# Performance work log

Hardware: AMD Instinct MI355X
Metric: run time of the kernel (lower is better)

## Reference

```python
import jax, jax.numpy as jnp
import numpy as np

B, L = 4096, 64          # batch, patch_len
OUT, KS, K = 64, 8, 4    # out_planes, kernel_size, num mixtures
STRIDE = 1
TEMP = 34.0
L_OUT = (L - KS) // STRIDE + 1   # 57
C = OUT * L_OUT                  # BN feature dim = 3648
HIDDEN = int(L * 0.5) + 1        # attention hidden planes = 33
EPS = 1e-5


def _gelu(x):
    return jax.nn.gelu(x, approximate=False)  # torch nn.GELU default = exact erf


def setup_inputs() -> dict:
    key = jax.random.key(0)
    ks = jax.random.split(key, 8)
    return {
        "x": jax.random.normal(ks[0], (B, L), jnp.float32),
        "fc1_w": jax.random.normal(ks[1], (HIDDEN, L), jnp.float32) * (2.0 / HIDDEN) ** 0.5,
        "fc2_w": jax.random.normal(ks[2], (K, HIDDEN), jnp.float32) * (2.0 / K) ** 0.5,
        "fc2_b": jnp.zeros((K,), jnp.float32),
        "weight": jax.random.normal(ks[3], (K, OUT, KS), jnp.float32) * 0.1,
        "bias": jnp.zeros((K, OUT), jnp.float32),
        "bn_gamma": jnp.ones((C,), jnp.float32),
        "bn_beta": jnp.zeros((C,), jnp.float32),
    }


def reference(x, fc1_w, fc2_w, fc2_b, weight, bias, bn_gamma, bn_beta):
    # --- attention1d: 1x1 convs over the patch_len 'channel' dim == linears ---
    a = _gelu(x @ fc1_w.T)                 # [B, HIDDEN]
    logits = a @ fc2_w.T + fc2_b           # [B, K]
    attn = jax.nn.softmax(logits / TEMP, axis=1)

    # --- sliding windows (im2col), shared by both conv paths ---
    idx = jnp.arange(L_OUT)[:, None] * STRIDE + jnp.arange(KS)[None, :]
    frames = x[:, idx]                     # [B, L_OUT, KS]

    # --- kernel_wise: full conv with each of the K kernels ---
    kw = jnp.einsum('blc,koc->bolk', frames, weight) + bias.T[None, :, None, :]  # [B,OUT,L_OUT,K]
    kw = kw.reshape(B, C, K)

    # --- per-sample aggregated kernel + grouped (per-sample) conv ---
    agg_w = jnp.einsum('bk,koc->boc', attn, weight)      # [B, OUT, KS]
    agg_b = attn @ bias                                  # [B, OUT]
    out = jnp.einsum('blc,boc->bol', frames, agg_w) + agg_b[:, :, None]  # [B,OUT,L_OUT]
    out = out.reshape(B, C)

    # --- BN(GELU(.)) with batch statistics (training-mode BatchNorm1d) ---
    g = _gelu(out)
    m = g.mean(axis=0)
    v = g.var(axis=0)
    out = (g - m) * jax.lax.rsqrt(v + EPS) * bn_gamma + bn_beta

    g2 = _gelu(kw)                                        # [B, C, K]
    m2 = g2.mean(axis=(0, 2), keepdims=True)
    v2 = g2.var(axis=(0, 2), keepdims=True)
    kw = (g2 - m2) * jax.lax.rsqrt(v2 + EPS) * bn_gamma[None, :, None] + bn_beta[None, :, None]

    return out, attn, kw.transpose(0, 2, 1)              # [B,C], [B,K], [B,K,C]
```

## Files before the change

kernel.cpp:

```cpp
#include <hip/hip_runtime.h>
#include <cstddef>

#define B_     4096
#define L_     64
#define OUT_   64
#define KS_    8
#define KK_    4
#define LOUT_  57
#define C_     3648
#define HID_   33
#define TEMP_  34.0f
#define EPS_   1e-5f
#define NCH_   128
#define SROWS_ 32
#define NB2_   32

typedef float f32x2 __attribute__((ext_vector_type(2)));

__device__ __forceinline__ f32x2 pk_fma(f32x2 a, f32x2 b, f32x2 c) {
    return __builtin_elementwise_fma(a, b, c);
}

__device__ __forceinline__ float gelu_f(float x) {
    float e = exp2f(-2.3022083f * x * fmaf(0.044715f * x, x, 1.0f));
    return x * __builtin_amdgcn_rcpf(1.0f + e);
}

__device__ __forceinline__ f32x2 gelu2(f32x2 x) {
    const f32x2 one = {1.f, 1.f};
    const f32x2 ca  = {0.044715f, 0.044715f};
    const f32x2 cb  = {-2.3022083f, -2.3022083f};
    f32x2 t = pk_fma(x * ca, x, one);
    f32x2 u = x * t * cb;
    f32x2 e = {exp2f(u.x), exp2f(u.y)};
    f32x2 d = e + one;
    f32x2 r = {__builtin_amdgcn_rcpf(d.x), __builtin_amdgcn_rcpf(d.y)};
    return x * r;
}

template<int ROWS>
__device__ __forceinline__ void stage_shifted(
    const float* __restrict__ x, int b0, int tid,
    float4 (*xs4)[ROWS][17])
{
    for (int idx = tid; idx < ROWS * 16; idx += 256) {
        int r = idx >> 4, t = idx & 15;
        const float4* xrow = (const float4*)(x + (size_t)(b0 + r) * L_);
        float4 a  = xrow[t];
        float4 bq = xrow[t < 15 ? t + 1 : 15];
        xs4[0][r][t] = a;
        xs4[1][r][t] = make_float4(a.y, a.z, a.w, bq.x);
        xs4[2][r][t] = make_float4(a.z, a.w, bq.x, bq.y);
        xs4[3][r][t] = make_float4(a.w, bq.x, bq.y, bq.z);
    }
}

__global__ __launch_bounds__(128) void attn_kernel(
    const float* __restrict__ x, const float* __restrict__ fc1_w,
    const float* __restrict__ fc2_w, const float* __restrict__ fc2_b,
    float* __restrict__ attn_out)
{
    __shared__ float fc1s[HID_][L_];
    __shared__ float fc2s[KK_][HID_];
    __shared__ float fc2bs[KK_];
    int tid = threadIdx.x;
    for (int i = tid; i < HID_ * L_; i += 128) fc1s[i / L_][i % L_] = fc1_w[i];
    for (int i = tid; i < KK_ * HID_; i += 128) fc2s[i / HID_][i % HID_] = fc2_w[i];
    if (tid < KK_) fc2bs[tid] = fc2_b[tid];
    __syncthreads();

    int b = blockIdx.x * 128 + tid;

    float xr[L_];
    const float4* xp = (const float4*)(x + (size_t)b * L_);
    #pragma unroll
    for (int i = 0; i < L_ / 4; ++i) {
        float4 v = xp[i];
        xr[4*i] = v.x; xr[4*i+1] = v.y; xr[4*i+2] = v.z; xr[4*i+3] = v.w;
    }
    float logit[KK_] = {0.f, 0.f, 0.f, 0.f};
    for (int h = 0; h < HID_; ++h) {
        const float4* fr = (const float4*)&fc1s[h][0];
        float acc = 0.f;
        #pragma unroll
        for (int i = 0; i < L_ / 4; ++i) {
            float4 wv = fr[i];
            acc = fmaf(xr[4*i],   wv.x, acc);
            acc = fmaf(xr[4*i+1], wv.y, acc);
            acc = fmaf(xr[4*i+2], wv.z, acc);
            acc = fmaf(xr[4*i+3], wv.w, acc);
        }
        float a = gelu_f(acc);
        #pragma unroll
        for (int k = 0; k < KK_; ++k) logit[k] = fmaf(a, fc2s[k][h], logit[k]);
    }
    float z[KK_];
    #pragma unroll
    for (int k = 0; k < KK_; ++k) z[k] = (logit[k] + fc2bs[k]) * (1.0f / TEMP_);
    float mx = fmaxf(fmaxf(z[0], z[1]), fmaxf(z[2], z[3]));
    float e[KK_]; float s = 0.f;
    #pragma unroll
    for (int k = 0; k < KK_; ++k) { e[k] = __expf(z[k] - mx); s += e[k]; }
    float inv = __builtin_amdgcn_rcpf(s);
    #pragma unroll
    for (int k = 0; k < KK_; ++k) attn_out[(size_t)b * KK_ + k] = e[k] * inv;
}

__global__ __launch_bounds__(256) void stats_kernel(
    const float* __restrict__ x, const float* __restrict__ weight,
    const float* __restrict__ bias, const float* __restrict__ attn,
    float* __restrict__ P, int use_partial)
{
    int cb = blockIdx.x;
    int chunk = blockIdx.y;
    int tid = threadIdx.x;
    int c = cb * 256 + tid;
    bool act = c < C_;
    int o = act ? (c / LOUT_) : 0;
    int l = act ? (c - o * LOUT_) : 0;
    int q = l >> 2, s = l & 3;

    f32x2 wp[KK_][4];
    float bk[KK_];
    #pragma unroll
    for (int k = 0; k < KK_; ++k) {
        bk[k] = bias[k * OUT_ + o];
        const float* wk = weight + (size_t)(k * OUT_ + o) * KS_;
        #pragma unroll
        for (int j = 0; j < 4; ++j) wp[k][j] = f32x2{wk[2*j], wk[2*j+1]};
    }

    __shared__ float4 xs4[4][SROWS_][17];
    __shared__ float at[SROWS_][KK_];

    int b0 = chunk * SROWS_;
    stage_shifted<SROWS_>(x, b0, tid, xs4);
    if (tid < SROWS_ * KK_) ((float*)at)[tid] = attn[(size_t)b0 * KK_ + tid];
    __syncthreads();

    float s1 = 0.f, s2 = 0.f;
    f32x2 t1v = {0.f, 0.f}, t2v = {0.f, 0.f};
    if (act) {
        const float4* base = &xs4[s][0][q];
        #pragma unroll 4
        for (int r = 0; r < SROWS_; ++r) {
            float4 A  = base[(size_t)r * 17];
            float4 Bv = base[(size_t)r * 17 + 1];
            f32x2 xp[4] = {{A.x, A.y}, {A.z, A.w}, {Bv.x, Bv.y}, {Bv.z, Bv.w}};
            float kv[KK_];
            #pragma unroll
            for (int k = 0; k < KK_; ++k) {
                f32x2 acc = {bk[k], 0.f};
                #pragma unroll
                for (int j = 0; j < 4; ++j) acc = pk_fma(xp[j], wp[k][j], acc);
                kv[k] = acc.x + acc.y;
            }
            float ov = at[r][0] * kv[0];
            ov = fmaf(at[r][1], kv[1], ov);
            ov = fmaf(at[r][2], kv[2], ov);
            ov = fmaf(at[r][3], kv[3], ov);
            float g = gelu_f(ov);
            s1 += g; s2 = fmaf(g, g, s2);
            f32x2 g01 = gelu2(f32x2{kv[0], kv[1]});
            f32x2 g23 = gelu2(f32x2{kv[2], kv[3]});
            t1v = t1v + g01 + g23;
            t2v = pk_fma(g01, g01, t2v);
            t2v = pk_fma(g23, g23, t2v);
        }
    }
    if (!act) return;
    float t1 = t1v.x + t1v.y, t2 = t2v.x + t2v.y;
    if (use_partial) {
        size_t base = (size_t)chunk * 4 * C_ + c;
        P[base]          = s1;
        P[base + C_]     = s2;
        P[base + 2 * C_] = t1;
        P[base + 3 * C_] = t2;
    } else {
        atomicAdd(&P[c], s1);
        atomicAdd(&P[C_ + c], s2);
        atomicAdd(&P[2 * C_ + c], t1);
        atomicAdd(&P[3 * C_ + c], t2);
    }
}

__global__ __launch_bounds__(256) void finalize_kernel(
    const float* __restrict__ P, const float* __restrict__ gamma,
    const float* __restrict__ beta, float* __restrict__ F, int use_partial)
{
    __shared__ float red[4][64];
    int t = threadIdx.x;
    int cl = t & 63;
    int s = t >> 6;
    int c = blockIdx.x * 64 + cl;
    float a = 0.f;
    if (use_partial) {
        for (int ch = 0; ch < NCH_; ++ch)
            a += P[((size_t)ch * 4 + s) * C_ + c];
    } else {
        a = P[(size_t)s * C_ + c];
    }
    red[s][cl] = a;
    __syncthreads();
    if (t < 64) {
        float a0 = red[0][cl], a1 = red[1][cl], a2 = red[2][cl], a3 = red[3][cl];
        float m  = a0 * (1.0f / B_);
        float v  = a1 * (1.0f / B_) - m * m;
        float rs = rsqrtf(v + EPS_);
        float m2 = a2 * (1.0f / (B_ * KK_));
        float v2 = a3 * (1.0f / (B_ * KK_)) - m2 * m2;
        float rs2 = rsqrtf(v2 + EPS_);
        float ga = gamma[c], be = beta[c];
        F[c]          = rs * ga;
        F[C_ + c]     = be - m * rs * ga;
        F[2 * C_ + c] = rs2 * ga;
        F[3 * C_ + c] = be - m2 * rs2 * ga;
    }
}

__global__ __launch_bounds__(256) void write_kernel(
    const float* __restrict__ x, const float* __restrict__ weight,
    const float* __restrict__ bias, const float* __restrict__ attn,
    const float* __restrict__ F,
    float* __restrict__ out0, float* __restrict__ kwout)
{
    int cc = blockIdx.x;
    int bg = blockIdx.y;
    int tid = threadIdx.x;
    int c = cc * 256 + tid;
    bool act = c < C_;
    int o = act ? (c / LOUT_) : 0;
    int l = act ? (c - o * LOUT_) : 0;
    int q = l >> 2, s = l & 3;

    f32x2 wp[KK_][4];
    float bk[KK_];
    #pragma unroll
    for (int k = 0; k < KK_; ++k) {
        bk[k] = bias[k * OUT_ + o];
        const float* wk = weight + (size_t)(k * OUT_ + o) * KS_;
        #pragma unroll
        for (int j = 0; j < 4; ++j) wp[k][j] = f32x2{wk[2*j], wk[2*j+1]};
    }
    float sA = 0.f, hA = 0.f, sK = 0.f, hK = 0.f;
    if (act) {
        sA = F[c]; hA = F[C_ + c]; sK = F[2 * C_ + c]; hK = F[3 * C_ + c];
    }
    f32x2 sk2 = {sK, sK}, hk2 = {hK, hK};

    __shared__ float4 xs4[4][NB2_][17];
    __shared__ float at[NB2_][KK_];
    int b0 = bg * NB2_;
    stage_shifted<NB2_>(x, b0, tid, xs4);
    if (tid < NB2_ * KK_) ((float*)at)[tid] = attn[(size_t)b0 * KK_ + tid];
    __syncthreads();

    if (!act) return;

    const float4* xbase = &xs4[s][0][q];
    #pragma unroll 4
    for (int r = 0; r < NB2_; ++r) {
        float4 A  = xbase[(size_t)r * 17];
        float4 Bv = xbase[(size_t)r * 17 + 1];
        f32x2 xp[4] = {{A.x, A.y}, {A.z, A.w}, {Bv.x, Bv.y}, {Bv.z, Bv.w}};
        float kv[KK_];
        #pragma unroll
        for (int k = 0; k < KK_; ++k) {
            f32x2 acc = {bk[k], 0.f};
            #pragma unroll
            for (int j = 0; j < 4; ++j) acc = pk_fma(xp[j], wp[k][j], acc);
            kv[k] = acc.x + acc.y;
        }
        float ov = at[r][0] * kv[0];
        ov = fmaf(at[r][1], kv[1], ov);
        ov = fmaf(at[r][2], kv[2], ov);
        ov = fmaf(at[r][3], kv[3], ov);
        int b = b0 + r;
        float g = gelu_f(ov);
        out0[(size_t)b * C_ + c] = fmaf(g, sA, hA);
        f32x2 g01 = gelu2(f32x2{kv[0], kv[1]});
        f32x2 g23 = gelu2(f32x2{kv[2], kv[3]});
        f32x2 r01 = pk_fma(g01, sk2, hk2);
        f32x2 r23 = pk_fma(g23, sk2, hk2);
        float* base = kwout + (size_t)b * KK_ * C_ + c;
        base[0]      = r01.x;
        base[C_]     = r01.y;
        base[2 * C_] = r23.x;
        base[3 * C_] = r23.y;
    }
}

extern "C" void kernel_launch(void* const* d_in, const int* in_sizes, int n_in,
                              void* d_out, int out_size, void* d_ws, size_t ws_size,
                              hipStream_t stream) {
    const float* x      = (const float*)d_in[0];
    const float* fc1_w  = (const float*)d_in[1];
    const float* fc2_w  = (const float*)d_in[2];
    const float* fc2_b  = (const float*)d_in[3];
    const float* weight = (const float*)d_in[4];
    const float* bias   = (const float*)d_in[5];
    const float* gamma  = (const float*)d_in[6];
    const float* beta   = (const float*)d_in[7];

    float* out  = (float*)d_out;
    float* out0 = out;
    float* attn = out + (size_t)B_ * C_;
    float* kwout = attn + (size_t)B_ * KK_;

    size_t need = (size_t)(NCH_ * 4 + 4) * C_ * sizeof(float);
    int use_partial = ws_size >= need;
    float* P = (float*)d_ws;
    float* F = P + (use_partial ? (size_t)NCH_ * 4 * C_ : (size_t)4 * C_);
    if (!use_partial)
        hipMemsetAsync(P, 0, 4 * C_ * sizeof(float), stream);

    attn_kernel<<<B_ / 128, 128, 0, stream>>>(x, fc1_w, fc2_w, fc2_b, attn);
    stats_kernel<<<dim3((C_ + 255) / 256, NCH_), 256, 0, stream>>>(
        x, weight, bias, attn, P, use_partial);
    finalize_kernel<<<C_ / 64, 256, 0, stream>>>(P, gamma, beta, F, use_partial);
    write_kernel<<<dim3((C_ + 255) / 256, B_ / NB2_), 256, 0, stream>>>(
        x, weight, bias, attn, F, out0, kwout);
}
```

Before: 143.3 us.

## Fuse attention, stats, finalize and write into one cooperative kernel

Replaces the four-kernel pipeline (attn, stats, finalize, write) with a single cooperative-launch kernel that uses grid-wide syncs between the phases. Attention is computed by one block per 64-row chunk, per-chunk partial BN sums are reduced by chunk 0, and the conv results are recomputed in the write phase. This removes three kernel launch boundaries and the separate launch overhead. In exchange the grid is limited to 960 blocks that must all be co-resident, the finalize phase runs on only 15 blocks, and three grid barriers serialize the phases. It falls back to the old path if cooperative launch is unavailable or fails.

```diff
diff --git a/kernel.cpp b/kernel.cpp
--- a/kernel.cpp
+++ b/kernel.cpp
@@ -1,5 +1,8 @@
 #include <hip/hip_runtime.h>
+#include <hip/hip_cooperative_groups.h>
 #include <cstddef>
+
+namespace cg = cooperative_groups;
 
 #define B_     4096
 #define L_     64
@@ -14,6 +17,9 @@
 #define NCH_   128
 #define SROWS_ 32
 #define NB2_   32
+#define CHUNKS_ 64
+#define RPC_    64
+#define SR_     16
 
 typedef float f32x2 __attribute__((ext_vector_type(2)));
 
@@ -55,6 +61,197 @@
     }
 }
 
+__global__ __launch_bounds__(256, 4) void fused_kernel(
+    const float* __restrict__ x, const float* __restrict__ fc1_w,
+    const float* __restrict__ fc2_w, const float* __restrict__ fc2_b,
+    const float* __restrict__ weight, const float* __restrict__ bias,
+    const float* __restrict__ gamma, const float* __restrict__ beta,
+    float* __restrict__ attn_out, float* __restrict__ out0,
+    float* __restrict__ kwout, float* __restrict__ P, float* __restrict__ F)
+{
+    cg::grid_group grid = cg::this_grid();
+    int cb = blockIdx.x;
+    int chunk = blockIdx.y;
+    int tid = threadIdx.x;
+    int b0c = chunk * RPC_;
+
+    if (cb == 0) {
+        int r = tid >> 2, j = tid & 3;
+        int b = b0c + r;
+        const float4* xr4 = (const float4*)(x + (size_t)b * L_);
+        float lg0 = 0.f, lg1 = 0.f, lg2 = 0.f, lg3 = 0.f;
+        for (int h = j; h < HID_; h += 4) {
+            const float4* f4 = (const float4*)(fc1_w + (size_t)h * L_);
+            float acc = 0.f;
+            #pragma unroll
+            for (int i = 0; i < 16; ++i) {
+                float4 xv = xr4[i], wv = f4[i];
+                acc = fmaf(xv.x, wv.x, acc); acc = fmaf(xv.y, wv.y, acc);
+                acc = fmaf(xv.z, wv.z, acc); acc = fmaf(xv.w, wv.w, acc);
+            }
+            float a = gelu_f(acc);
+            lg0 = fmaf(a, fc2_w[h],             lg0);
+            lg1 = fmaf(a, fc2_w[HID_ + h],      lg1);
+            lg2 = fmaf(a, fc2_w[2 * HID_ + h],  lg2);
+            lg3 = fmaf(a, fc2_w[3 * HID_ + h],  lg3);
+        }
+        lg0 += __shfl_xor(lg0, 1, 4); lg0 += __shfl_xor(lg0, 2, 4);
+        lg1 += __shfl_xor(lg1, 1, 4); lg1 += __shfl_xor(lg1, 2, 4);
+        lg2 += __shfl_xor(lg2, 1, 4); lg2 += __shfl_xor(lg2, 2, 4);
+        lg3 += __shfl_xor(lg3, 1, 4); lg3 += __shfl_xor(lg3, 2, 4);
+        if (j == 0) {
+            float z0 = (lg0 + fc2_b[0]) * (1.0f / TEMP_);
+            float z1 = (lg1 + fc2_b[1]) * (1.0f / TEMP_);
+            float z2 = (lg2 + fc2_b[2]) * (1.0f / TEMP_);
+            float z3 = (lg3 + fc2_b[3]) * (1.0f / TEMP_);
+            float mx = fmaxf(fmaxf(z0, z1), fmaxf(z2, z3));
+            float e0 = __expf(z0 - mx), e1 = __expf(z1 - mx);
+            float e2 = __expf(z2 - mx), e3 = __expf(z3 - mx);
+            float inv = __builtin_amdgcn_rcpf(e0 + e1 + e2 + e3);
+            ((float4*)attn_out)[b] = make_float4(e0*inv, e1*inv, e2*inv, e3*inv);
+        }
+    }
+
+    int c = cb * 256 + tid;
+    bool act = c < C_;
+    int o = act ? (c / LOUT_) : 0;
+    int l = act ? (c - o * LOUT_) : 0;
+    int q = l >> 2, s = l & 3;
+
+    f32x2 wp[KK_][4];
+    float bk[KK_];
+    #pragma unroll
+    for (int k = 0; k < KK_; ++k) {
+        bk[k] = bias[k * OUT_ + o];
+        const float* wk = weight + (size_t)(k * OUT_ + o) * KS_;
+        #pragma unroll
+        for (int j = 0; j < 4; ++j) wp[k][j] = f32x2{wk[2*j], wk[2*j+1]};
+    }
+
+    __shared__ float4 xs4[4][SR_][17];
+    __shared__ float at[RPC_][KK_];
+
+    grid.sync();
+
+    if (tid < RPC_) ((float4*)at)[tid] = ((const float4*)attn_out)[b0c + tid];
+
+    float s1 = 0.f, s2 = 0.f;
+    f32x2 t1v = {0.f, 0.f}, t2v = {0.f, 0.f};
+    for (int round = 0; round < RPC_ / SR_; ++round) {
+        __syncthreads();
+        stage_shifted<SR_>(x, b0c + round * SR_, tid, xs4);
+        __syncthreads();
+        if (act) {
+            const float4* base = &xs4[s][0][q];
+            #pragma unroll 4
+            for (int r = 0; r < SR_; ++r) {
+                float4 A  = base[(size_t)r * 17];
+                float4 Bv = base[(size_t)r * 17 + 1];
+                f32x2 xp[4] = {{A.x, A.y}, {A.z, A.w}, {Bv.x, Bv.y}, {Bv.z, Bv.w}};
+                float kv[KK_];
+                #pragma unroll
+                for (int k = 0; k < KK_; ++k) {
+                    f32x2 acc = {bk[k], 0.f};
+                    #pragma unroll
+                    for (int j = 0; j < 4; ++j) acc = pk_fma(xp[j], wp[k][j], acc);
+                    kv[k] = acc.x + acc.y;
+                }
+                int rr = round * SR_ + r;
+                float ov = at[rr][0] * kv[0];
+                ov = fmaf(at[rr][1], kv[1], ov);
+                ov = fmaf(at[rr][2], kv[2], ov);
+                ov = fmaf(at[rr][3], kv[3], ov);
+                float g = gelu_f(ov);
+                s1 += g; s2 = fmaf(g, g, s2);
+                f32x2 g01 = gelu2(f32x2{kv[0], kv[1]});
+                f32x2 g23 = gelu2(f32x2{kv[2], kv[3]});
+                t1v = t1v + g01 + g23;
+                t2v = pk_fma(g01, g01, t2v);
+                t2v = pk_fma(g23, g23, t2v);
+            }
+        }
+    }
+    if (act) {
+        size_t base = (size_t)chunk * 4 * C_ + c;
+        P[base]          = s1;
+        P[base + C_]     = s2;
+        P[base + 2 * C_] = t1v.x + t1v.y;
+        P[base + 3 * C_] = t2v.x + t2v.y;
+    }
+
+    grid.sync();
+
+    if (chunk == 0 && act) {
+        float a0 = 0.f, a1 = 0.f, a2 = 0.f, a3 = 0.f;
+        for (int ch = 0; ch < CHUNKS_; ++ch) {
+            size_t base = (size_t)ch * 4 * C_ + c;
+            a0 += P[base];
+            a1 += P[base + C_];
+            a2 += P[base + 2 * C_];
+            a3 += P[base + 3 * C_];
+        }
+        float m  = a0 * (1.0f / B_);
+        float v  = a1 * (1.0f / B_) - m * m;
+        float rs = rsqrtf(v + EPS_);
+        float m2 = a2 * (1.0f / (B_ * KK_));
+        float v2 = a3 * (1.0f / (B_ * KK_)) - m2 * m2;
+        float rs2 = rsqrtf(v2 + EPS_);
+        float ga = gamma[c], be = beta[c];
+        F[c]          = rs * ga;
+        F[C_ + c]     = be - m * rs * ga;
+        F[2 * C_ + c] = rs2 * ga;
+        F[3 * C_ + c] = be - m2 * rs2 * ga;
+    }
+
+    grid.sync();
+
+    float sA = 0.f, hA = 0.f, sK = 0.f, hK = 0.f;
+    if (act) {
+        sA = F[c]; hA = F[C_ + c]; sK = F[2 * C_ + c]; hK = F[3 * C_ + c];
+    }
+    f32x2 sk2 = {sK, sK}, hk2 = {hK, hK};
+
+    for (int round = 0; round < RPC_ / SR_; ++round) {
+        __syncthreads();
+        stage_shifted<SR_>(x, b0c + round * SR_, tid, xs4);
+        __syncthreads();
+        if (act) {
+            const float4* base = &xs4[s][0][q];
+            #pragma unroll 4
+            for (int r = 0; r < SR_; ++r) {
+                float4 A  = base[(size_t)r * 17];
+                float4 Bv = base[(size_t)r * 17 + 1];
+                f32x2 xp[4] = {{A.x, A.y}, {A.z, A.w}, {Bv.x, Bv.y}, {Bv.z, Bv.w}};
+                float kv[KK_];
+                #pragma unroll
+                for (int k = 0; k < KK_; ++k) {
+                    f32x2 acc = {bk[k], 0.f};
+                    #pragma unroll
+                    for (int j = 0; j < 4; ++j) acc = pk_fma(xp[j], wp[k][j], acc);
+                    kv[k] = acc.x + acc.y;
+                }
+                int rr = round * SR_ + r;
+                float ov = at[rr][0] * kv[0];
+                ov = fmaf(at[rr][1], kv[1], ov);
+                ov = fmaf(at[rr][2], kv[2], ov);
+                ov = fmaf(at[rr][3], kv[3], ov);
+                int b = b0c + rr;
+                float g = gelu_f(ov);
+                out0[(size_t)b * C_ + c] = fmaf(g, sA, hA);
+                f32x2 g01 = gelu2(f32x2{kv[0], kv[1]});
+                f32x2 g23 = gelu2(f32x2{kv[2], kv[3]});
+                f32x2 r01 = pk_fma(g01, sk2, hk2);
+                f32x2 r23 = pk_fma(g23, sk2, hk2);
+                float* pb = kwout + (size_t)b * KK_ * C_ + c;
+                pb[0]      = r01.x;
+                pb[C_]     = r01.y;
+                pb[2 * C_] = r23.x;
+                pb[3 * C_] = r23.y;
+            }
+        }
+    }
+}
+
 __global__ __launch_bounds__(128) void attn_kernel(
     const float* __restrict__ x, const float* __restrict__ fc1_w,
     const float* __restrict__ fc2_w, const float* __restrict__ fc2_b,
@@ -70,7 +267,6 @@
     __syncthreads();
 
     int b = blockIdx.x * 128 + tid;
-
     float xr[L_];
     const float4* xp = (const float4*)(x + (size_t)b * L_);
     #pragma unroll
@@ -307,6 +503,22 @@
     float* attn = out + (size_t)B_ * C_;
     float* kwout = attn + (size_t)B_ * KK_;
 
+    size_t need_f = (size_t)(CHUNKS_ * 4 + 4) * C_ * sizeof(float);
+    int coop = 0;
+    hipDeviceGetAttribute(&coop, hipDeviceAttributeCooperativeLaunch, 0);
+    if (coop && ws_size >= need_f) {
+        float* P = (float*)d_ws;
+        float* F = P + (size_t)CHUNKS_ * 4 * C_;
+        void* args[] = {
+            (void*)&x, (void*)&fc1_w, (void*)&fc2_w, (void*)&fc2_b,
+            (void*)&weight, (void*)&bias, (void*)&gamma, (void*)&beta,
+            (void*)&attn, (void*)&out0, (void*)&kwout, (void*)&P, (void*)&F
+        };
+        hipError_t e = hipLaunchCooperativeKernel(
+            (const void*)fused_kernel, dim3(15, CHUNKS_), dim3(256), args, 0, stream);
+        if (e == hipSuccess) return;
+    }
+
     size_t need = (size_t)(NCH_ * 4 + 4) * C_ * sizeof(float);
     int use_partial = ws_size >= need;
     float* P = (float*)d_ws;
```

New measurement: 388.7 us. +171.2%, slower.

## Split attention hidden units across four lanes and pad shifted LDS planes

Applied to the files above, without the earlier changes.

The attention kernel now gives each batch row to four threads. Each thread handles a strided subset of the 33 hidden units and reads fc1 and fc2 weights straight from global memory instead of staging them in shared memory. The partial logits are combined with width-4 shuffles, and one lane does the softmax with a vectorized store. Separately, the four shifted x planes in shared memory are padded by two float4 per plane to change the bank mapping between planes, likely to cut LDS bank conflicts in the stats and write kernels. The attention change raises parallelism to 64 blocks of 256 threads, at the cost of redundant x and weight reads from global memory or cache.

```diff
diff --git a/kernel.cpp b/kernel.cpp
--- a/kernel.cpp
+++ b/kernel.cpp
@@ -14,6 +14,7 @@
 #define NCH_   128
 #define SROWS_ 32
 #define NB2_   32
+#define PLANE_ (SROWS_ * 17 + 2)
 
 typedef float f32x2 __attribute__((ext_vector_type(2)));
 
@@ -38,72 +39,62 @@
     return x * r;
 }
 
-template<int ROWS>
-__device__ __forceinline__ void stage_shifted(
-    const float* __restrict__ x, int b0, int tid,
-    float4 (*xs4)[ROWS][17])
-{
-    for (int idx = tid; idx < ROWS * 16; idx += 256) {
+__device__ __forceinline__ void stage_shifted_p(
+    const float* __restrict__ x, int b0, int tid, float4* xs4, int plane)
+{
+    for (int idx = tid; idx < SROWS_ * 16; idx += 256) {
         int r = idx >> 4, t = idx & 15;
         const float4* xrow = (const float4*)(x + (size_t)(b0 + r) * L_);
         float4 a  = xrow[t];
         float4 bq = xrow[t < 15 ? t + 1 : 15];
-        xs4[0][r][t] = a;
-        xs4[1][r][t] = make_float4(a.y, a.z, a.w, bq.x);
-        xs4[2][r][t] = make_float4(a.z, a.w, bq.x, bq.y);
-        xs4[3][r][t] = make_float4(a.w, bq.x, bq.y, bq.z);
-    }
-}
-
-__global__ __launch_bounds__(128) void attn_kernel(
+        int base = r * 17 + t;
+        xs4[base]             = a;
+        xs4[plane + base]     = make_float4(a.y, a.z, a.w, bq.x);
+        xs4[2 * plane + base] = make_float4(a.z, a.w, bq.x, bq.y);
+        xs4[3 * plane + base] = make_float4(a.w, bq.x, bq.y, bq.z);
+    }
+}
+
+__global__ __launch_bounds__(256) void attn_kernel(
     const float* __restrict__ x, const float* __restrict__ fc1_w,
     const float* __restrict__ fc2_w, const float* __restrict__ fc2_b,
     float* __restrict__ attn_out)
 {
-    __shared__ float fc1s[HID_][L_];
-    __shared__ float fc2s[KK_][HID_];
-    __shared__ float fc2bs[KK_];
     int tid = threadIdx.x;
-    for (int i = tid; i < HID_ * L_; i += 128) fc1s[i / L_][i % L_] = fc1_w[i];
-    for (int i = tid; i < KK_ * HID_; i += 128) fc2s[i / HID_][i % HID_] = fc2_w[i];
-    if (tid < KK_) fc2bs[tid] = fc2_b[tid];
-    __syncthreads();
-
-    int b = blockIdx.x * 128 + tid;
-
-    float xr[L_];
-    const float4* xp = (const float4*)(x + (size_t)b * L_);
-    #pragma unroll
-    for (int i = 0; i < L_ / 4; ++i) {
-        float4 v = xp[i];
-        xr[4*i] = v.x; xr[4*i+1] = v.y; xr[4*i+2] = v.z; xr[4*i+3] = v.w;
-    }
-    float logit[KK_] = {0.f, 0.f, 0.f, 0.f};
-    for (int h = 0; h < HID_; ++h) {
-        const float4* fr = (const float4*)&fc1s[h][0];
+    int r = tid >> 2, j = tid & 3;
+    int b = blockIdx.x * 64 + r;
+    const float4* xr4 = (const float4*)(x + (size_t)b * L_);
+    float lg0 = 0.f, lg1 = 0.f, lg2 = 0.f, lg3 = 0.f;
+    for (int h = j; h < HID_; h += 4) {
+        const float4* f4 = (const float4*)(fc1_w + (size_t)h * L_);
         float acc = 0.f;
         #pragma unroll
-        for (int i = 0; i < L_ / 4; ++i) {
-            float4 wv = fr[i];
-            acc = fmaf(xr[4*i],   wv.x, acc);
-            acc = fmaf(xr[4*i+1], wv.y, acc);
-            acc = fmaf(xr[4*i+2], wv.z, acc);
-            acc = fmaf(xr[4*i+3], wv.w, acc);
+        for (int i = 0; i < 16; ++i) {
+            float4 xv = xr4[i], wv = f4[i];
+            acc = fmaf(xv.x, wv.x, acc); acc = fmaf(xv.y, wv.y, acc);
+            acc = fmaf(xv.z, wv.z, acc); acc = fmaf(xv.w, wv.w, acc);
         }
         float a = gelu_f(acc);
-        #pragma unroll
-        for (int k = 0; k < KK_; ++k) logit[k] = fmaf(a, fc2s[k][h], logit[k]);
-    }
-    float z[KK_];
-    #pragma unroll
-    for (int k = 0; k < KK_; ++k) z[k] = (logit[k] + fc2bs[k]) * (1.0f / TEMP_);
-    float mx = fmaxf(fmaxf(z[0], z[1]), fmaxf(z[2], z[3]));
-    float e[KK_]; float s = 0.f;
-    #pragma unroll
-    for (int k = 0; k < KK_; ++k) { e[k] = __expf(z[k] - mx); s += e[k]; }
-    float inv = __builtin_amdgcn_rcpf(s);
-    #pragma unroll
-    for (int k = 0; k < KK_; ++k) attn_out[(size_t)b * KK_ + k] = e[k] * inv;
+        lg0 = fmaf(a, fc2_w[h],             lg0);
+        lg1 = fmaf(a, fc2_w[HID_ + h],      lg1);
+        lg2 = fmaf(a, fc2_w[2 * HID_ + h],  lg2);
+        lg3 = fmaf(a, fc2_w[3 * HID_ + h],  lg3);
+    }
+    lg0 += __shfl_xor(lg0, 1, 4); lg0 += __shfl_xor(lg0, 2, 4);
+    lg1 += __shfl_xor(lg1, 1, 4); lg1 += __shfl_xor(lg1, 2, 4);
+    lg2 += __shfl_xor(lg2, 1, 4); lg2 += __shfl_xor(lg2, 2, 4);
+    lg3 += __shfl_xor(lg3, 1, 4); lg3 += __shfl_xor(lg3, 2, 4);
+    if (j == 0) {
+        float z0 = (lg0 + fc2_b[0]) * (1.0f / TEMP_);
+        float z1 = (lg1 + fc2_b[1]) * (1.0f / TEMP_);
+        float z2 = (lg2 + fc2_b[2]) * (1.0f / TEMP_);
+        float z3 = (lg3 + fc2_b[3]) * (1.0f / TEMP_);
+        float mx = fmaxf(fmaxf(z0, z1), fmaxf(z2, z3));
+        float e0 = __expf(z0 - mx), e1 = __expf(z1 - mx);
+        float e2 = __expf(z2 - mx), e3 = __expf(z3 - mx);
+        float inv = __builtin_amdgcn_rcpf(e0 + e1 + e2 + e3);
+        ((float4*)attn_out)[b] = make_float4(e0*inv, e1*inv, e2*inv, e3*inv);
+    }
 }
 
 __global__ __launch_bounds__(256) void stats_kernel(
@@ -130,22 +121,22 @@
         for (int j = 0; j < 4; ++j) wp[k][j] = f32x2{wk[2*j], wk[2*j+1]};
     }
 
-    __shared__ float4 xs4[4][SROWS_][17];
+    __shared__ float4 xs4[4 * PLANE_];
     __shared__ float at[SROWS_][KK_];
 
     int b0 = chunk * SROWS_;
-    stage_shifted<SROWS_>(x, b0, tid, xs4);
+    stage_shifted_p(x, b0, tid, xs4, PLANE_);
     if (tid < SROWS_ * KK_) ((float*)at)[tid] = attn[(size_t)b0 * KK_ + tid];
     __syncthreads();
 
     float s1 = 0.f, s2 = 0.f;
     f32x2 t1v = {0.f, 0.f}, t2v = {0.f, 0.f};
     if (act) {
-        const float4* base = &xs4[s][0][q];
+        const float4* base = &xs4[s * PLANE_ + q];
         #pragma unroll 4
         for (int r = 0; r < SROWS_; ++r) {
-            float4 A  = base[(size_t)r * 17];
-            float4 Bv = base[(size_t)r * 17 + 1];
+            float4 A  = base[r * 17];
+            float4 Bv = base[r * 17 + 1];
             f32x2 xp[4] = {{A.x, A.y}, {A.z, A.w}, {Bv.x, Bv.y}, {Bv.z, Bv.w}};
             float kv[KK_];
             #pragma unroll
@@ -248,20 +239,20 @@
     }
     f32x2 sk2 = {sK, sK}, hk2 = {hK, hK};
 
-    __shared__ float4 xs4[4][NB2_][17];
+    __shared__ float4 xs4[4 * PLANE_];
     __shared__ float at[NB2_][KK_];
     int b0 = bg * NB2_;
-    stage_shifted<NB2_>(x, b0, tid, xs4);
+    stage_shifted_p(x, b0, tid, xs4, PLANE_);
     if (tid < NB2_ * KK_) ((float*)at)[tid] = attn[(size_t)b0 * KK_ + tid];
     __syncthreads();
 
     if (!act) return;
 
-    const float4* xbase = &xs4[s][0][q];
+    const float4* xbase = &xs4[s * PLANE_ + q];
     #pragma unroll 4
     for (int r = 0; r < NB2_; ++r) {
-        float4 A  = xbase[(size_t)r * 17];
-        float4 Bv = xbase[(size_t)r * 17 + 1];
+        float4 A  = xbase[r * 17];
+        float4 Bv = xbase[r * 17 + 1];
         f32x2 xp[4] = {{A.x, A.y}, {A.z, A.w}, {Bv.x, Bv.y}, {Bv.z, Bv.w}};
         float kv[KK_];
         #pragma unroll
@@ -314,7 +305,7 @@
     if (!use_partial)
         hipMemsetAsync(P, 0, 4 * C_ * sizeof(float), stream);
 
-    attn_kernel<<<B_ / 128, 128, 0, stream>>>(x, fc1_w, fc2_w, fc2_b, attn);
+    attn_kernel<<<B_ / 64, 256, 0, stream>>>(x, fc1_w, fc2_w, fc2_b, attn);
     stats_kernel<<<dim3((C_ + 255) / 256, NCH_), 256, 0, stream>>>(
         x, weight, bias, attn, P, use_partial);
     finalize_kernel<<<C_ / 64, 256, 0, stream>>>(P, gamma, beta, F, use_partial);
```

Measured after the change: 143.0 us. About the same (-0.2%).
